# Optimization experiments

Measured on AMD Instinct MI355X. Metric: run time of the kernel, lower is better.

## Reference

```python
import jax, jax.numpy as jnp
import numpy as np

B, T, D, U = 32, 2048, 512, 512

def setup_inputs() -> dict:
    key = jax.random.key(0)
    ks = jax.random.split(key, 8)
    s = 0.02
    return {
        "query": jax.random.normal(ks[0], (B, D), dtype=jnp.float32),
        "values": jax.random.normal(ks[1], (B, T, D), dtype=jnp.float32),
        "W1_w": jax.random.normal(ks[2], (D, U), dtype=jnp.float32) * s,
        "W1_b": jnp.zeros((U,), dtype=jnp.float32),
        "W2_w": jax.random.normal(ks[3], (D, U), dtype=jnp.float32) * s,
        "W2_b": jnp.zeros((U,), dtype=jnp.float32),
        "V_w": jax.random.normal(ks[4], (U, 1), dtype=jnp.float32) * s,
        "V_b": jnp.zeros((1,), dtype=jnp.float32),
    }

def reference(query, values, W1_w, W1_b, W2_w, W2_b, V_w, V_b):
    # query: [B, D] -> [B, 1, U]; values: [B, T, D] -> [B, T, U]
    q_proj = (query @ W1_w + W1_b)[:, None, :]              # [B, 1, U]
    v_proj = jnp.einsum('btd,du->btu', values, W2_w) + W2_b  # [B, T, U]
    score = jnp.tanh(q_proj + v_proj) @ V_w + V_b            # [B, T, 1]
    attn = jax.nn.softmax(score, axis=1)                     # [B, T, 1]
    context = jnp.sum(attn * values, axis=1)                 # [B, D]
    return context, attn
```

## Files before the change

### kernel.cpp

```cpp
#include <hip/hip_runtime.h>
#include <hip/hip_bf16.h>
#include <cstddef>
#include <cstdint>

#define B_ 32
#define T_ 2048
#define D_ 512
#define U_ 512

typedef __attribute__((ext_vector_type(8))) short bf16x8;
typedef __attribute__((ext_vector_type(4))) float f32x4;

__device__ __forceinline__ unsigned short f2bf(float f) {
  union { float f; unsigned u; } x; x.f = f;
  unsigned r = x.u + 0x7fffu + ((x.u >> 16) & 1u);
  return (unsigned short)(r >> 16);
}
__device__ __forceinline__ float tanh_fast(float x) {
  float e = __expf(2.0f * x);
  return 1.0f - 2.0f * __builtin_amdgcn_rcpf(e + 1.0f);
}

__device__ __forceinline__ void wave0_sumabs_vw(const float* __restrict__ Vw,
                                                float* Cs, int tid) {
  if (tid < 64) {
    float c = 0.f;
    #pragma unroll
    for (int i = 0; i < 8; ++i) c += fabsf(Vw[tid + i * 64]);
    c += __shfl_xor(c, 1);  c += __shfl_xor(c, 2);  c += __shfl_xor(c, 4);
    c += __shfl_xor(c, 8);  c += __shfl_xor(c, 16); c += __shfl_xor(c, 32);
    if (tid == 0) *Cs = c;
  }
}

__global__ void kA_prep(const float* __restrict__ W2, unsigned* __restrict__ W2P,
                        const float* __restrict__ query, const float* __restrict__ W1,
                        const float* __restrict__ W1b, const float* __restrict__ W2b,
                        float* __restrict__ qp, float* __restrict__ ctx) {
  const int tid = threadIdx.x;
  if (blockIdx.x < 16) {
    const int kg = blockIdx.x;
    __shared__ unsigned short w2s[32][514];
    const float4* W2v = (const float4*)(W2 + (size_t)kg * 32 * U_);
    #pragma unroll
    for (int i = 0; i < 16; ++i) {
      int idx = i * 256 + tid;
      float4 v = W2v[idx];
      int r = idx >> 7, c = (idx & 127) * 4;
      w2s[r][c + 0] = f2bf(v.x); w2s[r][c + 1] = f2bf(v.y);
      w2s[r][c + 2] = f2bf(v.z); w2s[r][c + 3] = f2bf(v.w);
    }
    __syncthreads();
    const int lq = tid >> 6, lr = (tid >> 2) & 15, j = tid & 3;
    const int kb = lq * 8 + j * 2;
    #pragma unroll
    for (int ut = 0; ut < 32; ++ut)
      W2P[ut * 4096 + kg * 256 + tid] =
          (unsigned)w2s[kb][ut * 16 + lr] | ((unsigned)w2s[kb + 1][ut * 16 + lr] << 16);
  } else {
    __shared__ float qs[D_];
    const int blk = blockIdx.x - 16;
    const int b = blk >> 1, uhh = (blk & 1) * 256;
    qs[tid] = query[b * D_ + tid];
    qs[tid + 256] = query[b * D_ + tid + 256];
    __syncthreads();
    const int u = uhh + tid;
    float a0 = 0, a1 = 0, a2 = 0, a3 = 0, a4 = 0, a5 = 0, a6 = 0, a7 = 0;
    for (int d = 0; d < D_; d += 8) {
      a0 += qs[d + 0] * W1[(size_t)(d + 0) * U_ + u];
      a1 += qs[d + 1] * W1[(size_t)(d + 1) * U_ + u];
      a2 += qs[d + 2] * W1[(size_t)(d + 2) * U_ + u];
      a3 += qs[d + 3] * W1[(size_t)(d + 3) * U_ + u];
      a4 += qs[d + 4] * W1[(size_t)(d + 4) * U_ + u];
      a5 += qs[d + 5] * W1[(size_t)(d + 5) * U_ + u];
      a6 += qs[d + 6] * W1[(size_t)(d + 6) * U_ + u];
      a7 += qs[d + 7] * W1[(size_t)(d + 7) * U_ + u];
    }
    qp[b * U_ + u] = ((a0 + a1) + (a2 + a3)) + ((a4 + a5) + (a6 + a7)) + W1b[u] + W2b[u];
    const int gt = blk * 256 + tid;
    ctx[gt] = 0.0f;
  }
}

__global__ __launch_bounds__(512, 4) void k2attn(
    const float* __restrict__ values, const unsigned short* __restrict__ W2P,
    const float* __restrict__ qp, const float* __restrict__ Vw,
    float* __restrict__ score, float* __restrict__ ctxU) {
  __shared__ __align__(16) float avb[4][1024];
  __shared__ float sred[8][32];
  __shared__ float ps2[32];
  __shared__ float Cs;

  const int tid = threadIdx.x;
  const int bx = blockIdx.x;
  const int m0 = bx * 32;
  const int b = m0 >> 11;
  const int l = tid & 63, w = tid >> 6;
  const int lr = l & 15, lq = l >> 4;

  const int row_st = w * 4 + (l >> 4);
  const int fseg = l & 15;
  const float* vrow = values + (size_t)(m0 + row_st) * D_ + fseg * 4;

  f32x4 acc[2][4];
  #pragma unroll
  for (int mi = 0; mi < 2; ++mi)
    #pragma unroll
    for (int ni = 0; ni < 4; ++ni) acc[mi][ni] = (f32x4){0.f, 0.f, 0.f, 0.f};

  const unsigned short* Bb = W2P + (size_t)(w * 4) * 8192 + (size_t)l * 8;

  auto consume = [&](float4 g, int s) {
    __hip_bfloat162 h0 = __float22bfloat162_rn(make_float2(g.x, g.y));
    __hip_bfloat162 h1 = __float22bfloat162_rn(make_float2(g.z, g.w));
    union { __hip_bfloat162 h; unsigned u; } c0, c1; c0.h = h0; c1.h = h1;
    int slot = (fseg >> 1) ^ (row_st & 7);
    char* dst = (char*)avb[s & 3] + row_st * 128 + (slot << 4) + ((fseg & 1) << 3);
    *(uint2*)dst = make_uint2(c0.u, c1.u);
  };

  bf16x8 Bf[3][4];
  auto loadB = [&](int slot, int kappa) {
    #pragma unroll
    for (int ni = 0; ni < 4; ++ni)
      Bf[slot][ni] = *(const bf16x8*)(Bb + (size_t)ni * 8192 + (size_t)kappa * 512);
  };

  wave0_sumabs_vw(Vw, &Cs, tid);

  float4 g0 = *(const float4*)(vrow);
  float4 g1 = *(const float4*)(vrow + 64);
  float4 g2 = *(const float4*)(vrow + 128);
  float4 g3 = *(const float4*)(vrow + 192);
  loadB(0, 0);
  loadB(1, 1);
  consume(g0, 0);
  consume(g1, 1);
  __syncthreads();
  const float C = Cs;
  float4 Gpend[2];
  Gpend[0] = g2; Gpend[1] = g3;

  #pragma unroll
  for (int e = 0; e < 8; ++e) {
    float4 Gnew = (float4){0.f, 0.f, 0.f, 0.f};
    if (e < 4) Gnew = *(const float4*)(vrow + (e + 4) * 64);
    const char* buf = (const char*)avb[e & 3];
    #pragma unroll
    for (int kq = 0; kq < 2; ++kq) {
      const int kappa = e * 2 + kq;
      if (kappa + 2 < 16) loadB((kappa + 2) % 3, kappa + 2);
      const int sl = ((kq << 2) | lq) ^ (lr & 7);
      bf16x8 a0 = *(const bf16x8*)(buf + (lr) * 128 + (sl << 4));
      bf16x8 a1 = *(const bf16x8*)(buf + (16 + lr) * 128 + (sl << 4));
      __builtin_amdgcn_s_setprio(1);
      acc[0][0] = __builtin_amdgcn_mfma_f32_16x16x32_bf16(a0, Bf[kappa % 3][0], acc[0][0], 0, 0, 0);
      acc[1][0] = __builtin_amdgcn_mfma_f32_16x16x32_bf16(a1, Bf[kappa % 3][0], acc[1][0], 0, 0, 0);
      acc[0][1] = __builtin_amdgcn_mfma_f32_16x16x32_bf16(a0, Bf[kappa % 3][1], acc[0][1], 0, 0, 0);
      acc[1][1] = __builtin_amdgcn_mfma_f32_16x16x32_bf16(a1, Bf[kappa % 3][1], acc[1][1], 0, 0, 0);
      acc[0][2] = __builtin_amdgcn_mfma_f32_16x16x32_bf16(a0, Bf[kappa % 3][2], acc[0][2], 0, 0, 0);
      acc[1][2] = __builtin_amdgcn_mfma_f32_16x16x32_bf16(a1, Bf[kappa % 3][2], acc[1][2], 0, 0, 0);
      acc[0][3] = __builtin_amdgcn_mfma_f32_16x16x32_bf16(a0, Bf[kappa % 3][3], acc[0][3], 0, 0, 0);
      acc[1][3] = __builtin_amdgcn_mfma_f32_16x16x32_bf16(a1, Bf[kappa % 3][3], acc[1][3], 0, 0, 0);
      __builtin_amdgcn_s_setprio(0);
      if (kq == 0 && e < 6) consume(Gpend[0], e + 2);
    }
    Gpend[0] = Gpend[1]; Gpend[1] = Gnew;
    if (e & 1) {
      __builtin_amdgcn_sched_barrier(0);
      asm volatile("s_waitcnt lgkmcnt(0)" ::: "memory");
      __builtin_amdgcn_s_barrier();
      __builtin_amdgcn_sched_barrier(0);
    }
  }

  float sacc[2][4];
  #pragma unroll
  for (int mi = 0; mi < 2; ++mi)
    #pragma unroll
    for (int r = 0; r < 4; ++r) sacc[mi][r] = 0.0f;
  #pragma unroll
  for (int ni = 0; ni < 4; ++ni) {
    int u = (w * 4 + ni) * 16 + lr;
    float qpv = qp[b * U_ + u], vv = Vw[u];
    #pragma unroll
    for (int mi = 0; mi < 2; ++mi)
      #pragma unroll
      for (int r = 0; r < 4; ++r)
        sacc[mi][r] += tanh_fast(acc[mi][ni][r] + qpv) * vv;
  }
  #pragma unroll
  for (int mi = 0; mi < 2; ++mi)
    #pragma unroll
    for (int r = 0; r < 4; ++r) {
      float v = sacc[mi][r];
      v += __shfl_xor(v, 1); v += __shfl_xor(v, 2);
      v += __shfl_xor(v, 4); v += __shfl_xor(v, 8);
      if (lr == 0) sred[w][mi * 16 + lq * 4 + r] = v;
    }
  __syncthreads();

  if (tid < 32) {
    float s = 0.f;
    #pragma unroll
    for (int wv = 0; wv < 8; ++wv) s += sred[wv][tid];
    score[m0 + tid] = s;
    ps2[tid] = __expf(s - C);
  }
  __syncthreads();

  float accc = 0.f;
  const int col = tid;
  #pragma unroll 4
  for (int row = 0; row < 32; ++row)
    accc += ps2[row] * values[(size_t)(m0 + row) * D_ + col];
  atomicAdd(&ctxU[(size_t)b * D_ + col], accc);
}

__global__ void kB_final(const float* __restrict__ Vw, float* __restrict__ attn,
                         float* __restrict__ ctx) {
  __shared__ float Cs;
  __shared__ float red[4];
  const int b = blockIdx.x, tid = threadIdx.x;
  wave0_sumabs_vw(Vw, &Cs, tid);
  __syncthreads();
  const float C = Cs;
  float* s = attn + b * T_;
  float p[8];
  float sum = 0.f;
  #pragma unroll
  for (int i = 0; i < 8; ++i) { p[i] = __expf(s[tid + i * 256] - C); sum += p[i]; }
  #pragma unroll
  for (int off = 1; off < 64; off <<= 1) sum += __shfl_xor(sum, off);
  if ((tid & 63) == 0) red[tid >> 6] = sum;
  __syncthreads();
  sum = (red[0] + red[1]) + (red[2] + red[3]);
  const float inv = 1.0f / sum;
  #pragma unroll
  for (int i = 0; i < 8; ++i) attn[b * T_ + tid + i * 256] = p[i] * inv;
  #pragma unroll
  for (int i = 0; i < 2; ++i) ctx[b * D_ + tid + i * 256] *= inv;
}

extern "C" void kernel_launch(void* const* d_in, const int* in_sizes, int n_in,
                              void* d_out, int out_size, void* d_ws, size_t ws_size,
                              hipStream_t stream) {
  const float* query = (const float*)d_in[0];
  const float* values = (const float*)d_in[1];
  const float* W1w = (const float*)d_in[2];
  const float* W1b = (const float*)d_in[3];
  const float* W2w = (const float*)d_in[4];
  const float* W2b = (const float*)d_in[5];
  const float* Vw  = (const float*)d_in[6];

  float* out = (float*)d_out;
  float* ctx  = out;
  float* attn = out + B_ * D_;
  float* score = attn;

  char* ws = (char*)d_ws;
  unsigned* W2P = (unsigned*)ws;
  float* qp    = (float*)(ws + 512 * 1024);

  kA_prep<<<80, 256, 0, stream>>>(W2w, W2P, query, W1w, W1b, W2b, qp, ctx);
  k2attn<<<2048, 512, 0, stream>>>(values, (const unsigned short*)W2P, qp, Vw, score, ctx);
  kB_final<<<32, 256, 0, stream>>>(Vw, attn, ctx);
}
```

Measured before the change: 267.4 us.

## Stage values via async global-to-LDS loads with 64-row, 1024-thread attention blocks

The main attention kernel now uses 1024-thread blocks that each cover 64 rows. Values are copied straight into a triple-buffered fp32 LDS ring with global_load_lds, and conversion to bf16 happens after the LDS read, right before the MFMAs. Two halves of the block share the same W2 fragments, and their context partials are combined in LDS before one atomic per column. The prep kernel is split across more blocks to spread the W2 packing and query projection. The aim is to remove the register round-trip for values and to halve the atomics and W2 fragment loads per row, at the cost of more LDS (48KB fp32 staging) and hand-tuned vmcnt waits that may limit occupancy.

```diff
diff --git a/kernel.cpp b/kernel.cpp
--- a/kernel.cpp
+++ b/kernel.cpp
@@ -20,6 +20,9 @@
   float e = __expf(2.0f * x);
   return 1.0f - 2.0f * __builtin_amdgcn_rcpf(e + 1.0f);
 }
+
+#define AS1C(p) ((const __attribute__((address_space(1))) unsigned*)(p))
+#define AS3(p)  ((__attribute__((address_space(3))) unsigned*)(p))
 
 __device__ __forceinline__ void wave0_sumabs_vw(const float* __restrict__ Vw,
                                                 float* Cs, int tid) {
@@ -38,69 +41,77 @@
                         const float* __restrict__ W1b, const float* __restrict__ W2b,
                         float* __restrict__ qp, float* __restrict__ ctx) {
   const int tid = threadIdx.x;
-  if (blockIdx.x < 16) {
-    const int kg = blockIdx.x;
-    __shared__ unsigned short w2s[32][514];
-    const float4* W2v = (const float4*)(W2 + (size_t)kg * 32 * U_);
-    #pragma unroll
-    for (int i = 0; i < 16; ++i) {
-      int idx = i * 256 + tid;
-      float4 v = W2v[idx];
-      int r = idx >> 7, c = (idx & 127) * 4;
+  if (blockIdx.x < 64) {
+    const int kg = blockIdx.x >> 2, q4 = blockIdx.x & 3;
+    __shared__ unsigned short w2s[8][514];
+    const float4* W2v = (const float4*)(W2 + (size_t)(kg * 32 + q4 * 8) * U_);
+    #pragma unroll
+    for (int i = 0; i < 4; ++i) {
+      int idx4 = i * 256 + tid;
+      float4 v = W2v[idx4];
+      int r = idx4 >> 7, c = (idx4 & 127) * 4;
       w2s[r][c + 0] = f2bf(v.x); w2s[r][c + 1] = f2bf(v.y);
       w2s[r][c + 2] = f2bf(v.z); w2s[r][c + 3] = f2bf(v.w);
     }
     __syncthreads();
-    const int lq = tid >> 6, lr = (tid >> 2) & 15, j = tid & 3;
-    const int kb = lq * 8 + j * 2;
-    #pragma unroll
-    for (int ut = 0; ut < 32; ++ut)
-      W2P[ut * 4096 + kg * 256 + tid] =
+    const int idx = tid & 63;
+    const int lr = (idx >> 2) & 15, j = idx & 3;
+    const int kb = j * 2;
+    #pragma unroll
+    for (int r = 0; r < 8; ++r) {
+      int ut = r * 4 + (tid >> 6);
+      W2P[ut * 4096 + kg * 256 + q4 * 64 + idx] =
           (unsigned)w2s[kb][ut * 16 + lr] | ((unsigned)w2s[kb + 1][ut * 16 + lr] << 16);
+    }
   } else {
     __shared__ float qs[D_];
-    const int blk = blockIdx.x - 16;
-    const int b = blk >> 1, uhh = (blk & 1) * 256;
+    __shared__ float red[4][64];
+    const int blk2 = blockIdx.x - 64;
+    const int b = blk2 >> 3, us = blk2 & 7;
+    const int ul = tid & 63, dq = tid >> 6;
+    const int u = us * 64 + ul;
     qs[tid] = query[b * D_ + tid];
     qs[tid + 256] = query[b * D_ + tid + 256];
     __syncthreads();
-    const int u = uhh + tid;
-    float a0 = 0, a1 = 0, a2 = 0, a3 = 0, a4 = 0, a5 = 0, a6 = 0, a7 = 0;
-    for (int d = 0; d < D_; d += 8) {
-      a0 += qs[d + 0] * W1[(size_t)(d + 0) * U_ + u];
-      a1 += qs[d + 1] * W1[(size_t)(d + 1) * U_ + u];
-      a2 += qs[d + 2] * W1[(size_t)(d + 2) * U_ + u];
-      a3 += qs[d + 3] * W1[(size_t)(d + 3) * U_ + u];
-      a4 += qs[d + 4] * W1[(size_t)(d + 4) * U_ + u];
-      a5 += qs[d + 5] * W1[(size_t)(d + 5) * U_ + u];
-      a6 += qs[d + 6] * W1[(size_t)(d + 6) * U_ + u];
-      a7 += qs[d + 7] * W1[(size_t)(d + 7) * U_ + u];
-    }
-    qp[b * U_ + u] = ((a0 + a1) + (a2 + a3)) + ((a4 + a5) + (a6 + a7)) + W1b[u] + W2b[u];
-    const int gt = blk * 256 + tid;
-    ctx[gt] = 0.0f;
-  }
-}
-
-__global__ __launch_bounds__(512, 4) void k2attn(
+    float a0 = 0, a1 = 0, a2 = 0, a3 = 0;
+    const int d0 = dq * 128;
+    for (int d = 0; d < 128; d += 4) {
+      a0 += qs[d0 + d + 0] * W1[(size_t)(d0 + d + 0) * U_ + u];
+      a1 += qs[d0 + d + 1] * W1[(size_t)(d0 + d + 1) * U_ + u];
+      a2 += qs[d0 + d + 2] * W1[(size_t)(d0 + d + 2) * U_ + u];
+      a3 += qs[d0 + d + 3] * W1[(size_t)(d0 + d + 3) * U_ + u];
+    }
+    red[dq][ul] = (a0 + a1) + (a2 + a3);
+    __syncthreads();
+    if (dq == 0) {
+      float s = red[0][ul] + red[1][ul] + red[2][ul] + red[3][ul];
+      qp[b * U_ + u] = s + W1b[u] + W2b[u];
+    }
+    if (tid < 64) ctx[blk2 * 64 + tid] = 0.0f;
+  }
+}
+
+__global__ __launch_bounds__(1024, 4) void k2attn(
     const float* __restrict__ values, const unsigned short* __restrict__ W2P,
     const float* __restrict__ qp, const float* __restrict__ Vw,
     float* __restrict__ score, float* __restrict__ ctxU) {
-  __shared__ __align__(16) float avb[4][1024];
-  __shared__ float sred[8][32];
-  __shared__ float ps2[32];
+  __shared__ __align__(16) float av[3][4096];
+  __shared__ float sred[16][32];
+  __shared__ float ps2[64];
+  __shared__ float pc[512];
   __shared__ float Cs;
 
   const int tid = threadIdx.x;
   const int bx = blockIdx.x;
-  const int m0 = bx * 32;
+  const int m0 = bx * 64;
   const int b = m0 >> 11;
   const int l = tid & 63, w = tid >> 6;
   const int lr = l & 15, lq = l >> 4;
-
-  const int row_st = w * 4 + (l >> 4);
-  const int fseg = l & 15;
-  const float* vrow = values + (size_t)(m0 + row_st) * D_ + fseg * 4;
+  const int h = w >> 3, uw = w & 7;
+
+  const int row_g = w * 4 + (l >> 4);
+  const int qsw = (l & 15) ^ (row_g & 15);
+  const float* vsrc = values + (size_t)(m0 + row_g) * D_ + qsw * 4;
 
   f32x4 acc[2][4];
   #pragma unroll
@@ -108,17 +119,11 @@
     #pragma unroll
     for (int ni = 0; ni < 4; ++ni) acc[mi][ni] = (f32x4){0.f, 0.f, 0.f, 0.f};
 
-  const unsigned short* Bb = W2P + (size_t)(w * 4) * 8192 + (size_t)l * 8;
-
-  auto consume = [&](float4 g, int s) {
-    __hip_bfloat162 h0 = __float22bfloat162_rn(make_float2(g.x, g.y));
-    __hip_bfloat162 h1 = __float22bfloat162_rn(make_float2(g.z, g.w));
-    union { __hip_bfloat162 h; unsigned u; } c0, c1; c0.h = h0; c1.h = h1;
-    int slot = (fseg >> 1) ^ (row_st & 7);
-    char* dst = (char*)avb[s & 3] + row_st * 128 + (slot << 4) + ((fseg & 1) << 3);
-    *(uint2*)dst = make_uint2(c0.u, c1.u);
+  const unsigned short* Bb = W2P + (size_t)(uw * 4) * 8192 + (size_t)l * 8;
+
+  auto stage = [&](int s) {
+    __builtin_amdgcn_global_load_lds(AS1C(vsrc + s * 64), AS3(&av[s % 3][w * 256]), 16, 0, 0);
   };
-
   bf16x8 Bf[3][4];
   auto loadB = [&](int slot, int kappa) {
     #pragma unroll
@@ -128,47 +133,48 @@
 
   wave0_sumabs_vw(Vw, &Cs, tid);
 
-  float4 g0 = *(const float4*)(vrow);
-  float4 g1 = *(const float4*)(vrow + 64);
-  float4 g2 = *(const float4*)(vrow + 128);
-  float4 g3 = *(const float4*)(vrow + 192);
   loadB(0, 0);
   loadB(1, 1);
-  consume(g0, 0);
-  consume(g1, 1);
-  __syncthreads();
+  stage(0);
+  stage(1);
+  __builtin_amdgcn_sched_barrier(0);
+  asm volatile("s_waitcnt vmcnt(1) lgkmcnt(0)" ::: "memory");
+  __builtin_amdgcn_s_barrier();
+  __builtin_amdgcn_sched_barrier(0);
   const float C = Cs;
-  float4 Gpend[2];
-  Gpend[0] = g2; Gpend[1] = g3;
 
   #pragma unroll
   for (int e = 0; e < 8; ++e) {
-    float4 Gnew = (float4){0.f, 0.f, 0.f, 0.f};
-    if (e < 4) Gnew = *(const float4*)(vrow + (e + 4) * 64);
-    const char* buf = (const char*)avb[e & 3];
+    const float* buf = (const float*)av[e % 3];
     #pragma unroll
     for (int kq = 0; kq < 2; ++kq) {
       const int kappa = e * 2 + kq;
       if (kappa + 2 < 16) loadB((kappa + 2) % 3, kappa + 2);
-      const int sl = ((kq << 2) | lq) ^ (lr & 7);
-      bf16x8 a0 = *(const bf16x8*)(buf + (lr) * 128 + (sl << 4));
-      bf16x8 a1 = *(const bf16x8*)(buf + (16 + lr) * 128 + (sl << 4));
-      __builtin_amdgcn_s_setprio(1);
-      acc[0][0] = __builtin_amdgcn_mfma_f32_16x16x32_bf16(a0, Bf[kappa % 3][0], acc[0][0], 0, 0, 0);
-      acc[1][0] = __builtin_amdgcn_mfma_f32_16x16x32_bf16(a1, Bf[kappa % 3][0], acc[1][0], 0, 0, 0);
-      acc[0][1] = __builtin_amdgcn_mfma_f32_16x16x32_bf16(a0, Bf[kappa % 3][1], acc[0][1], 0, 0, 0);
-      acc[1][1] = __builtin_amdgcn_mfma_f32_16x16x32_bf16(a1, Bf[kappa % 3][1], acc[1][1], 0, 0, 0);
-      acc[0][2] = __builtin_amdgcn_mfma_f32_16x16x32_bf16(a0, Bf[kappa % 3][2], acc[0][2], 0, 0, 0);
-      acc[1][2] = __builtin_amdgcn_mfma_f32_16x16x32_bf16(a1, Bf[kappa % 3][2], acc[1][2], 0, 0, 0);
-      acc[0][3] = __builtin_amdgcn_mfma_f32_16x16x32_bf16(a0, Bf[kappa % 3][3], acc[0][3], 0, 0, 0);
-      acc[1][3] = __builtin_amdgcn_mfma_f32_16x16x32_bf16(a1, Bf[kappa % 3][3], acc[1][3], 0, 0, 0);
-      __builtin_amdgcn_s_setprio(0);
-      if (kq == 0 && e < 6) consume(Gpend[0], e + 2);
-    }
-    Gpend[0] = Gpend[1]; Gpend[1] = Gnew;
-    if (e & 1) {
       __builtin_amdgcn_sched_barrier(0);
-      asm volatile("s_waitcnt lgkmcnt(0)" ::: "memory");
+      const int p0 = (kq * 8 + lq * 2) ^ lr;
+      #pragma unroll
+      for (int mi = 0; mi < 2; ++mi) {
+        const int row = h * 32 + mi * 16 + lr;
+        f32x4 flo = *(const f32x4*)&buf[row * 64 + (p0 << 2)];
+        f32x4 fhi = *(const f32x4*)&buf[row * 64 + ((p0 ^ 1) << 2)];
+        union { bf16x8 v; __hip_bfloat162 hh[4]; } A;
+        A.hh[0] = __float22bfloat162_rn(make_float2(flo.x, flo.y));
+        A.hh[1] = __float22bfloat162_rn(make_float2(flo.z, flo.w));
+        A.hh[2] = __float22bfloat162_rn(make_float2(fhi.x, fhi.y));
+        A.hh[3] = __float22bfloat162_rn(make_float2(fhi.z, fhi.w));
+        __builtin_amdgcn_s_setprio(1);
+        acc[mi][0] = __builtin_amdgcn_mfma_f32_16x16x32_bf16(A.v, Bf[kappa % 3][0], acc[mi][0], 0, 0, 0);
+        acc[mi][1] = __builtin_amdgcn_mfma_f32_16x16x32_bf16(A.v, Bf[kappa % 3][1], acc[mi][1], 0, 0, 0);
+        acc[mi][2] = __builtin_amdgcn_mfma_f32_16x16x32_bf16(A.v, Bf[kappa % 3][2], acc[mi][2], 0, 0, 0);
+        acc[mi][3] = __builtin_amdgcn_mfma_f32_16x16x32_bf16(A.v, Bf[kappa % 3][3], acc[mi][3], 0, 0, 0);
+        __builtin_amdgcn_s_setprio(0);
+      }
+    }
+    if (e + 2 < 8) stage(e + 2);
+    __builtin_amdgcn_sched_barrier(0);
+    if (e < 7) {
+      if (e == 6) asm volatile("s_waitcnt vmcnt(8)" ::: "memory");
+      else        asm volatile("s_waitcnt vmcnt(9)" ::: "memory");
       __builtin_amdgcn_s_barrier();
       __builtin_amdgcn_sched_barrier(0);
     }
@@ -181,7 +187,7 @@
     for (int r = 0; r < 4; ++r) sacc[mi][r] = 0.0f;
   #pragma unroll
   for (int ni = 0; ni < 4; ++ni) {
-    int u = (w * 4 + ni) * 16 + lr;
+    int u = (uw * 4 + ni) * 16 + lr;
     float qpv = qp[b * U_ + u], vv = Vw[u];
     #pragma unroll
     for (int mi = 0; mi < 2; ++mi)
@@ -200,21 +206,24 @@
     }
   __syncthreads();
 
-  if (tid < 32) {
+  if (tid < 64) {
+    const int hh = tid >> 5, loc = tid & 31;
     float s = 0.f;
     #pragma unroll
-    for (int wv = 0; wv < 8; ++wv) s += sred[wv][tid];
+    for (int j = 0; j < 8; ++j) s += sred[hh * 8 + j][loc];
     score[m0 + tid] = s;
     ps2[tid] = __expf(s - C);
   }
   __syncthreads();
 
+  const int col = tid & 511, rh = tid >> 9;
   float accc = 0.f;
-  const int col = tid;
   #pragma unroll 4
   for (int row = 0; row < 32; ++row)
-    accc += ps2[row] * values[(size_t)(m0 + row) * D_ + col];
-  atomicAdd(&ctxU[(size_t)b * D_ + col], accc);
+    accc += ps2[rh * 32 + row] * values[(size_t)(m0 + rh * 32 + row) * D_ + col];
+  if (rh == 1) pc[col] = accc;
+  __syncthreads();
+  if (rh == 0) atomicAdd(&ctxU[(size_t)b * D_ + col], accc + pc[col]);
 }
 
 __global__ void kB_final(const float* __restrict__ Vw, float* __restrict__ attn,
@@ -262,7 +271,7 @@
   unsigned* W2P = (unsigned*)ws;
   float* qp    = (float*)(ws + 512 * 1024);
 
-  kA_prep<<<80, 256, 0, stream>>>(W2w, W2P, query, W1w, W1b, W2b, qp, ctx);
-  k2attn<<<2048, 512, 0, stream>>>(values, (const unsigned short*)W2P, qp, Vw, score, ctx);
+  kA_prep<<<320, 256, 0, stream>>>(W2w, W2P, query, W1w, W1b, W2b, qp, ctx);
+  k2attn<<<1024, 1024, 0, stream>>>(values, (const unsigned short*)W2P, qp, Vw, score, ctx);
   kB_final<<<32, 256, 0, stream>>>(Vw, attn, ctx);
 }
```

Measured after the change: 268.5 us. About the same (+0.4%).
